# Performance work log

Measured on AMD Instinct MI355X. Metric: run time of the kernel, lower is better.

Reference implementation:

```python
import jax, jax.numpy as jnp
import numpy as np

D_MODEL = 1024
NUM_HEADS = 16
D_K = D_MODEL // NUM_HEADS
B, T = 2, 2048


def setup_inputs() -> dict:
    key = jax.random.key(0)
    ks = jax.random.split(key, 11)
    s = 1.0 / np.sqrt(D_MODEL)
    inp = {
        "q": jax.random.normal(ks[0], (B, T, D_MODEL), jnp.float32),
        "k": jax.random.normal(ks[1], (B, T, D_MODEL), jnp.float32),
        "v": jax.random.normal(ks[2], (B, T, D_MODEL), jnp.float32),
        "mask": jnp.tril(jnp.ones((1, 1, T, T), jnp.int32)),  # causal
        "wq": jax.random.normal(ks[3], (D_MODEL, D_MODEL), jnp.float32) * s,
        "bq": jnp.zeros((D_MODEL,), jnp.float32),
        "wk": jax.random.normal(ks[4], (D_MODEL, D_MODEL), jnp.float32) * s,
        "bk": jnp.zeros((D_MODEL,), jnp.float32),
        "wv": jax.random.normal(ks[5], (D_MODEL, D_MODEL), jnp.float32) * s,
        "bv": jnp.zeros((D_MODEL,), jnp.float32),
        "wo": jax.random.normal(ks[6], (D_MODEL, D_MODEL), jnp.float32) * s,
        "bo": jnp.zeros((D_MODEL,), jnp.float32),
    }
    return inp


def reference(q, k, v, mask, wq, bq, wk, bk, wv, bv, wo, bo):
    Bq, Tq, _ = q.shape
    Tk = k.shape[1]
    # projections, split into heads: (B, H, T, d_k)
    qh = (q @ wq + bq).reshape(Bq, Tq, NUM_HEADS, D_K).transpose(0, 2, 1, 3)
    kh = (k @ wk + bk).reshape(Bq, Tk, NUM_HEADS, D_K).transpose(0, 2, 1, 3)
    vh = (v @ wv + bv).reshape(Bq, Tk, NUM_HEADS, D_K).transpose(0, 2, 1, 3)
    scores = jnp.einsum("bhqd,bhkd->bhqk", qh, kh) / jnp.sqrt(jnp.float32(D_K))
    scores = jnp.where(mask == 0, jnp.float32(-1e9), scores)
    attn = jax.nn.softmax(scores, axis=-1)
    ctx = jnp.einsum("bhqk,bhkd->bhqd", attn, vh)
    ctx = ctx.transpose(0, 2, 1, 3).reshape(Bq, Tq, D_MODEL)
    return ctx @ wo + bo
```

## Files before the change

### kernel.cpp

```cpp
#include <hip/hip_runtime.h>
#include <hip/hip_bf16.h>

#define DM 1024
#define NH 16
#define DK 64
#define TT 2048
#define BATCH 2

typedef __attribute__((ext_vector_type(8))) short bf16x8;
typedef __attribute__((ext_vector_type(4))) float f32x4;
typedef __attribute__((ext_vector_type(4))) unsigned short u16x4;
typedef unsigned short u16;

__device__ inline u16 f2b(float x){ __hip_bfloat16 h = __float2bfloat16(x); return *reinterpret_cast<u16*>(&h); }

__device__ inline void gl_lds16(const u16* g, u16* l) {
  __builtin_amdgcn_global_load_lds(
      (const __attribute__((address_space(1))) unsigned int*)g,
      (__attribute__((address_space(3))) unsigned int*)l, 16, 0, 0);
}

__global__ __launch_bounds__(256) void prep(const float* __restrict__ q, const float* __restrict__ k,
                                            const float* __restrict__ v,
                                            const float* __restrict__ wq, const float* __restrict__ wk,
                                            const float* __restrict__ wv, const float* __restrict__ wo,
                                            u16* __restrict__ qb, u16* __restrict__ kb,
                                            u16* __restrict__ vb, u16* __restrict__ wt) {
  int z = blockIdx.z;
  if (z < 3) {
    const float* src = z==0 ? q : z==1 ? k : v;
    u16* dst = z==0 ? qb : z==1 ? kb : vb;
    size_t i = ((size_t)blockIdx.x*256 + threadIdx.x)*8;
    f32x4 a = *(const f32x4*)(src+i);
    f32x4 b = *(const f32x4*)(src+i+4);
    union { bf16x8 v8; u16 e[8]; } u;
    #pragma unroll
    for (int j=0;j<4;j++){ u.e[j] = f2b(a[j]); u.e[4+j] = f2b(b[j]); }
    *(bf16x8*)(dst+i) = u.v8;
  } else {
    int bx = blockIdx.x;
    if (bx >= 1024) return;
    __shared__ float tile[32][33];
    const float* src = z==3 ? wq : z==4 ? wk : z==5 ? wv : wo;
    u16* dst = wt + (size_t)(z-3)*DM*DM;
    int bxx = bx & 31, byy = bx >> 5;
    int tx = threadIdx.x & 31, ty = threadIdx.x >> 5;
    int x  = bxx*32 + tx;
    int y0 = byy*32 + ty;
    #pragma unroll
    for (int i=0;i<32;i+=8) tile[ty+i][tx] = src[(size_t)(y0+i)*DM + x];
    __syncthreads();
    int xo = byy*32 + tx;
    int yo = bxx*32 + ty;
    #pragma unroll
    for (int i=0;i<32;i+=8) dst[(size_t)(yo+i)*DM + xo] = f2b(tile[tx][ty+i]);
  }
}

__global__ __launch_bounds__(512, 2) void gemm_qkv(const u16* __restrict__ qb, const u16* __restrict__ kb,
                                                   const u16* __restrict__ vb, const u16* __restrict__ wt,
                                                   const float* __restrict__ bq, const float* __restrict__ bk,
                                                   const float* __restrict__ bv,
                                                   u16* __restrict__ qh, u16* __restrict__ kh,
                                                   u16* __restrict__ vhT) {
  const int bid = blockIdx.x;
  const int swz = (bid & 7)*24 + (bid >> 3);
  const int z  = swz >> 6;
  const int rb = swz & 63;
  const int row0 = (rb >> 2) * 256;
  const int col0 = (rb & 3) * 256;

  const u16* A = z==0 ? qb : z==1 ? kb : vb;
  const u16* W = wt + (size_t)z*DM*DM;
  const float* bias = z==0 ? bq : z==1 ? bk : bv;
  u16* outv = z==0 ? qh : z==1 ? kh : vhT;
  const int mode = (z==2);
  const float oscale = (z==0) ? 0.18033688f : 1.0f;

  __shared__ __align__(16) u16 As[2][16384];
  __shared__ __align__(16) u16 Bs[2][16384];

  const int tid = threadIdx.x, lane = tid & 63, wid = tid >> 6;
  const int li = lane & 15, quad = lane >> 4, l7 = lane & 7;
  const int wr = wid >> 2, wc = wid & 3;

  int r_[2], gs_[2];
  #pragma unroll
  for (int c=0;c<2;c++){ int idx = tid + c*512; int rr = idx>>3; int gd = idx&7; r_[c]=rr; gs_[c]=gd^(rr&7); }

  auto stage = [&](int op, int t, int hf, int slot){
    const u16* base = op ? W : A;
    const int rowbase = (op ? col0 : row0) + hf*128;
    u16* lb = (op ? Bs[slot] : As[slot]) + hf*8192;
    #pragma unroll
    for (int c=0;c<2;c++){
      gl_lds16(base + (size_t)(rowbase + r_[c])*DM + t*64 + gs_[c]*8,
               lb + ((wid*64 + c*512) << 3));
    }
  };

  f32x4 acc[8][4];
  #pragma unroll
  for (int i=0;i<8;i++)
    #pragma unroll
    for (int j=0;j<4;j++) acc[i][j] = f32x4{0.f,0.f,0.f,0.f};

  stage(1, 0, 0, 0); stage(1, 0, 1, 0);
  stage(0, 0, 0, 0); stage(0, 0, 1, 0);
  stage(1, 1, 0, 1); stage(1, 1, 1, 1);
  asm volatile("s_waitcnt vmcnt(4)" ::: "memory");
  __builtin_amdgcn_s_barrier();

  bf16x8 b[4][2];
  for (int i = 0; i < 8; i++) {
    const int t2 = 2*i;
    #pragma unroll
    for (int half = 0; half < 2; half++) {
      const int slot = half;
      #pragma unroll
      for (int q = 0; q < 4; q++) {
        if (q == 0) {
          const u16* bb = Bs[slot] + (wc>>1)*8192 + (wc&1)*4096;
          #pragma unroll
          for (int c=0;c<4;c++)
            #pragma unroll
            for (int kh=0;kh<2;kh++)
              b[c][kh] = *(const bf16x8*)&bb[(c*16 + li)*64 + ((quad + 4*kh) ^ l7)*8];
        }
        bf16x8 a[2][2];
        {
          const u16* ab = As[slot] + wr*8192;
          #pragma unroll
          for (int rr2=0; rr2<2; rr2++)
            #pragma unroll
            for (int kh=0;kh<2;kh++)
              a[rr2][kh] = *(const bf16x8*)&ab[((q*2+rr2)*16 + li)*64 + ((quad + 4*kh) ^ l7)*8];
        }
        {
          const int sop = (q >= 2);
          const int st  = t2 + 1 + half + (q >= 2);
          const int shf = q & 1;
          const int ssl = (q >= 2) ? half : (1 - half);
          if (st <= 15) stage(sop, st, shf, ssl);
        }
        if (q == 0) asm volatile("s_waitcnt lgkmcnt(8)" ::: "memory");
        __builtin_amdgcn_s_barrier();
        asm volatile("s_waitcnt lgkmcnt(0)" ::: "memory");
        __builtin_amdgcn_sched_barrier(0);
        __builtin_amdgcn_s_setprio(1);
        #pragma unroll
        for (int rr2=0; rr2<2; rr2++)
          #pragma unroll
          for (int c=0;c<4;c++)
            #pragma unroll
            for (int kh=0;kh<2;kh++)
              acc[q*2+rr2][c] = __builtin_amdgcn_mfma_f32_16x16x32_bf16(a[rr2][kh], b[c][kh], acc[q*2+rr2][c], 0,0,0);
        __builtin_amdgcn_s_setprio(0);
        if (q == 3) {
          if (half == 0) {
            if (i < 7) asm volatile("s_waitcnt vmcnt(4)" ::: "memory");
            else       asm volatile("s_waitcnt vmcnt(0)" ::: "memory");
          } else {
            if (i < 7) asm volatile("s_waitcnt vmcnt(4)" ::: "memory");
          }
        }
        __builtin_amdgcn_s_barrier();
      }
    }
  }

  if (!mode) {
    #pragma unroll
    for (int c=0;c<4;c++) {
      int col = col0 + wc*64 + c*16 + li;
      float bsv = bias[col];
      #pragma unroll
      for (int fr=0; fr<8; fr++) {
        int rowb = row0 + wr*128 + fr*16 + quad*4;
        #pragma unroll
        for (int r=0;r<4;r++)
          outv[(size_t)(rowb + r)*DM + col] = f2b((acc[fr][c][r] + bsv) * oscale);
      }
    }
  } else {
    #pragma unroll
    for (int c=0;c<4;c++) {
      int col = col0 + wc*64 + c*16 + li;
      float bsv = bias[col];
      int hh = col >> 6, d = col & 63;
      #pragma unroll
      for (int fr=0; fr<8; fr++) {
        int rowb = row0 + wr*128 + fr*16 + quad*4;
        int bb = rowb >> 11, t0 = rowb & (TT-1);
        u16x4 w;
        #pragma unroll
        for (int r=0;r<4;r++) w[r] = f2b(acc[fr][c][r] + bsv);
        *(u16x4*)&outv[(((size_t)(bb*NH + hh)*DK + d)*TT) + t0] = w;
      }
    }
  }
}

__global__ __launch_bounds__(256) void gemm_out64(const u16* __restrict__ A, const u16* __restrict__ W,
                                                  const float* __restrict__ bias, float* __restrict__ out) {
  __shared__ __align__(16) u16 As[3][128*32];
  __shared__ __align__(16) u16 Bs[3][64*32];
  const int tid = threadIdx.x, lane = tid & 63, wid = tid >> 6;
  const int li = lane & 15, quad = lane >> 4;
  const int row0 = blockIdx.x*128, col0 = blockIdx.y*64;
  const int wr = wid & 1, wc = wid >> 1;

  const int srow = lane >> 2;
  const int scol = ((lane & 3) ^ ((srow >> 1) & 3)) * 8;
  const int rsw  = (li >> 1) & 3;

  auto stage = [&](int hh, int bufi) {
    const int kk = hh*32;
    #pragma unroll
    for (int c=0;c<2;c++) {
      int ch = wid*2 + c;
      gl_lds16(A + (size_t)(row0 + ch*16 + srow)*DM + kk + scol, &As[bufi][ch*512]);
    }
    gl_lds16(W + (size_t)(col0 + wid*16 + srow)*DM + kk + scol, &Bs[bufi][wid*512]);
  };

  f32x4 acc[4][2];
  #pragma unroll
  for (int i=0;i<4;i++)
    #pragma unroll
    for (int j=0;j<2;j++) acc[i][j] = f32x4{0.f,0.f,0.f,0.f};

  stage(0, 0);
  stage(1, 1);
  asm volatile("s_waitcnt vmcnt(3)" ::: "memory");
  __builtin_amdgcn_s_barrier();

  int buf = 0;
  for (int h = 0; h < 32; h++) {
    bf16x8 a[4], b[2];
    #pragma unroll
    for (int i=0;i<4;i++) a[i] = *(const bf16x8*)&As[buf][(wr*64 + i*16 + li)*32 + (quad ^ rsw)*8];
    #pragma unroll
    for (int j=0;j<2;j++) b[j] = *(const bf16x8*)&Bs[buf][(wc*32 + j*16 + li)*32 + (quad ^ rsw)*8];

    if (h < 30) { int nb = buf + 2; if (nb >= 3) nb -= 3; stage(h+2, nb); }

    __builtin_amdgcn_s_setprio(1);
    #pragma unroll
    for (int i=0;i<4;i++)
      #pragma unroll
      for (int j=0;j<2;j++)
        acc[i][j] = __builtin_amdgcn_mfma_f32_16x16x32_bf16(a[i], b[j], acc[i][j], 0,0,0);
    __builtin_amdgcn_s_setprio(0);

    if (h < 30)       asm volatile("s_waitcnt vmcnt(3)" ::: "memory");
    else if (h == 30) asm volatile("s_waitcnt vmcnt(0)" ::: "memory");
    __builtin_amdgcn_s_barrier();
    if (++buf == 3) buf = 0;
  }

  #pragma unroll
  for (int j=0;j<2;j++) {
    int col = col0 + wc*32 + j*16 + li;
    float bsv = bias[col];
    #pragma unroll
    for (int i=0;i<4;i++) {
      #pragma unroll
      for (int r=0;r<4;r++) {
        int row = row0 + wr*64 + i*16 + quad*4 + r;
        out[(size_t)row*DM + col] = acc[i][j][r] + bsv;
      }
    }
  }
}

__global__ __launch_bounds__(256) void flash(const u16* __restrict__ qh, const u16* __restrict__ kh,
                                             const u16* __restrict__ vhT, u16* __restrict__ ctx) {
  const int bh = blockIdx.x;
  const int y  = blockIdx.y;
  const int qt = (y < 8) ? (15 - y) : (y - 8);
  const int b = bh >> 4, h = bh & 15;
  const u16* Q  = qh  + (size_t)b*TT*DM + h*DK;
  const u16* K  = kh  + (size_t)b*TT*DM + h*DK;
  const u16* Vt = vhT + (size_t)bh*DK*TT;

  const int tid = threadIdx.x, lane = tid & 63, wid = tid >> 6;
  const int li = lane & 15, quad = lane >> 4, l7 = lane & 7;

  __shared__ __align__(16) u16 Pb[4][16][64];

  const int qw0 = qt*128 + wid*32;
  const int ntw = (qw0 + 31)/64 + 1;

  bf16x8 qf[2][2];
  #pragma unroll
  for (int su=0; su<2; su++)
    #pragma unroll
    for (int k2=0; k2<2; k2++)
      qf[su][k2] = *(const bf16x8*)&Q[(size_t)(qw0 + su*16 + li)*DM + k2*32 + quad*8];

  f32x4 o[2][4];
  #pragma unroll
  for (int su=0; su<2; su++)
    #pragma unroll
    for (int d=0; d<4; d++) o[su][d] = f32x4{0.f,0.f,0.f,0.f};
  float lp[2] = {0.f, 0.f};

  for (int n = 0; n < ntw; n++) {
    const int k0 = n*64;

    f32x4 sacc[2][4];
    #pragma unroll
    for (int c=0;c<4;c++) {
      const u16* krow = &K[(size_t)(k0 + c*16 + li)*DM];
      bf16x8 kf0 = *(const bf16x8*)&krow[     quad*8];
      bf16x8 kf1 = *(const bf16x8*)&krow[32 + quad*8];
      #pragma unroll
      for (int su=0; su<2; su++) {
        f32x4 t = __builtin_amdgcn_mfma_f32_16x16x32_bf16(kf0, qf[su][0], f32x4{0.f,0.f,0.f,0.f}, 0,0,0);
        sacc[su][c] = __builtin_amdgcn_mfma_f32_16x16x32_bf16(kf1, qf[su][1], t, 0,0,0);
      }
    }

    bf16x8 vf[4][2];
    #pragma unroll
    for (int d=0; d<4; d++) {
      const u16* vrow = &Vt[(size_t)(d*16 + li)*TT + k0];
      vf[d][0] = *(const bf16x8*)&vrow[     quad*8];
      vf[d][1] = *(const bf16x8*)&vrow[32 + quad*8];
    }

    const bool dg = (k0 + 63 > qw0);
    #pragma unroll
    for (int su=0; su<2; su++) {
      const int qr = qw0 + su*16;
      if (k0 <= qr + 15) {
        const int qq = qr + li;
        float p[4][4];
        if (dg) {
          #pragma unroll
          for (int c=0;c<4;c++)
            #pragma unroll
            for (int r=0;r<4;r++){
              int key = k0 + c*16 + quad*4 + r;
              p[c][r] = (key <= qq) ? exp2f(sacc[su][c][r]) : 0.f;
            }
        } else {
          #pragma unroll
          for (int c=0;c<4;c++)
            #pragma unroll
            for (int r=0;r<4;r++)
              p[c][r] = exp2f(sacc[su][c][r]);
        }
        #pragma unroll
        for (int c=0;c<4;c++)
          #pragma unroll
          for (int r=0;r<4;r++)
            lp[su] += p[c][r];

        #pragma unroll
        for (int c=0;c<4;c++) {
          u16x4 wv;
          #pragma unroll
          for (int r=0;r<4;r++) wv[r] = f2b(p[c][r]);
          const int gc = c*2 + (quad>>1);
          *(u16x4*)&Pb[wid][li][((gc ^ l7)*8) + (quad&1)*4] = wv;
        }
        __builtin_amdgcn_wave_barrier();
        __asm__ __volatile__("s_waitcnt lgkmcnt(0)");
        bf16x8 pf0 = *(const bf16x8*)&Pb[wid][li][((quad    ) ^ l7)*8];
        bf16x8 pf1 = *(const bf16x8*)&Pb[wid][li][((quad + 4) ^ l7)*8];
        __asm__ __volatile__("s_waitcnt lgkmcnt(0)");

        #pragma unroll
        for (int d=0;d<4;d++){
          o[su][d] = __builtin_amdgcn_mfma_f32_16x16x32_bf16(vf[d][0], pf0, o[su][d], 0,0,0);
          o[su][d] = __builtin_amdgcn_mfma_f32_16x16x32_bf16(vf[d][1], pf1, o[su][d], 0,0,0);
        }
      }
    }
  }

  #pragma unroll
  for (int su=0; su<2; su++) {
    float lpv = lp[su];
    lpv += __shfl_xor(lpv, 16, 64);
    lpv += __shfl_xor(lpv, 32, 64);
    float rl = 1.0f / lpv;
    const int qq = qw0 + su*16 + li;
    #pragma unroll
    for (int d=0;d<4;d++){
      u16x4 wv;
      #pragma unroll
      for (int r=0;r<4;r++) wv[r] = f2b(o[su][d][r] * rl);
      *(u16x4*)&ctx[(size_t)(b*TT + qq)*DM + h*DK + d*16 + quad*4] = wv;
    }
  }
}

extern "C" void kernel_launch(void* const* d_in, const int* in_sizes, int n_in,
                              void* d_out, int out_size, void* d_ws, size_t ws_size,
                              hipStream_t stream) {
  const float* q   = (const float*)d_in[0];
  const float* k   = (const float*)d_in[1];
  const float* v   = (const float*)d_in[2];
  const float* wq  = (const float*)d_in[4];
  const float* bq  = (const float*)d_in[5];
  const float* wk  = (const float*)d_in[6];
  const float* bk  = (const float*)d_in[7];
  const float* wv  = (const float*)d_in[8];
  const float* bv  = (const float*)d_in[9];
  const float* wo  = (const float*)d_in[10];
  const float* bo  = (const float*)d_in[11];
  float* out = (float*)d_out;

  const size_t SZ = (size_t)BATCH*TT*DM;
  u16* wt  = (u16*)d_ws;
  u16* qb  = wt + (size_t)4*DM*DM;
  u16* kb  = qb + SZ;
  u16* vb  = kb + SZ;
  u16* qh  = vb + SZ;
  u16* kh  = qh + SZ;
  u16* vhT = kh + SZ;
  u16* ctx = qb;

  prep<<<dim3(2048, 1, 7), 256, 0, stream>>>(q, k, v, wq, wk, wv, wo, qb, kb, vb, wt);

  gemm_qkv<<<dim3(192, 1, 1), 512, 0, stream>>>(qb, kb, vb, wt, bq, bk, bv, qh, kh, vhT);

  flash<<<dim3(BATCH*NH, 16), 256, 0, stream>>>(qh, kh, vhT, ctx);

  gemm_out64<<<dim3(4096/128, DM/64), 256, 0, stream>>>(ctx, wt + (size_t)3*DM*DM, bo, out);
}
```

Before: 246.2 us.

## Stage K/V tiles in double-buffered LDS and halve flash query tile

The flash kernel now cooperatively loads each 64-key K and V^T tile into swizzled, double-buffered shared memory, prefetching the next tile into registers while computing. All four waves read from LDS instead of each issuing redundant global loads. Each wave now handles 16 query rows instead of 32, with 64-row query tiles and twice as many blocks, and MFMA sections are wrapped in s_setprio. This trades a block-wide __syncthreads per tile and extra LDS for less global traffic and better load balance.

```diff
diff --git a/kernel.cpp b/kernel.cpp
--- a/kernel.cpp
+++ b/kernel.cpp
@@ -278,7 +278,7 @@
                                              const u16* __restrict__ vhT, u16* __restrict__ ctx) {
   const int bh = blockIdx.x;
   const int y  = blockIdx.y;
-  const int qt = (y < 8) ? (15 - y) : (y - 8);
+  const int qt = (y < 16) ? (31 - y) : (y - 16);
   const int b = bh >> 4, h = bh & 15;
   const u16* Q  = qh  + (size_t)b*TT*DM + h*DK;
   const u16* K  = kh  + (size_t)b*TT*DM + h*DK;
@@ -287,114 +287,114 @@
   const int tid = threadIdx.x, lane = tid & 63, wid = tid >> 6;
   const int li = lane & 15, quad = lane >> 4, l7 = lane & 7;
 
+  __shared__ __align__(16) u16 Kl[2][4096];
+  __shared__ __align__(16) u16 Vl[2][4096];
   __shared__ __align__(16) u16 Pb[4][16][64];
 
-  const int qw0 = qt*128 + wid*32;
-  const int ntw = (qw0 + 31)/64 + 1;
-
-  bf16x8 qf[2][2];
-  #pragma unroll
-  for (int su=0; su<2; su++)
-    #pragma unroll
-    for (int k2=0; k2<2; k2++)
-      qf[su][k2] = *(const bf16x8*)&Q[(size_t)(qw0 + su*16 + li)*DM + k2*32 + quad*8];
-
-  f32x4 o[2][4];
-  #pragma unroll
-  for (int su=0; su<2; su++)
-    #pragma unroll
-    for (int d=0; d<4; d++) o[su][d] = f32x4{0.f,0.f,0.f,0.f};
-  float lp[2] = {0.f, 0.f};
-
-  for (int n = 0; n < ntw; n++) {
+  const int sr = tid >> 3;
+  const int sg = tid & 7;
+  const int ssl = (sg ^ (sr & 7)) * 8;
+
+  const int nt  = qt + 1;
+  const int qw0 = qt*64 + wid*16;
+
+  bf16x8 qf0 = *(const bf16x8*)&Q[(size_t)(qw0 + li)*DM +      quad*8];
+  bf16x8 qf1 = *(const bf16x8*)&Q[(size_t)(qw0 + li)*DM + 32 + quad*8];
+
+  f32x4 o[4];
+  #pragma unroll
+  for (int d=0; d<4; d++) o[d] = f32x4{0.f,0.f,0.f,0.f};
+  float lp = 0.f;
+
+  bf16x8 kr0 = *(const bf16x8*)&K[(size_t)(sr   )*DM + sg*8];
+  bf16x8 kr1 = *(const bf16x8*)&K[(size_t)(sr+32)*DM + sg*8];
+  bf16x8 vr0 = *(const bf16x8*)&Vt[(size_t)(sr   )*TT + sg*8];
+  bf16x8 vr1 = *(const bf16x8*)&Vt[(size_t)(sr+32)*TT + sg*8];
+
+  for (int n = 0; n < nt; n++) {
     const int k0 = n*64;
-
-    f32x4 sacc[2][4];
+    const int s = n & 1;
+    *(bf16x8*)&Kl[s][(sr   )*64 + ssl] = kr0;
+    *(bf16x8*)&Kl[s][(sr+32)*64 + ssl] = kr1;
+    *(bf16x8*)&Vl[s][(sr   )*64 + ssl] = vr0;
+    *(bf16x8*)&Vl[s][(sr+32)*64 + ssl] = vr1;
+    __syncthreads();
+    if (n+1 < nt) {
+      const int k1 = k0 + 64;
+      kr0 = *(const bf16x8*)&K[(size_t)(k1+sr   )*DM + sg*8];
+      kr1 = *(const bf16x8*)&K[(size_t)(k1+sr+32)*DM + sg*8];
+      vr0 = *(const bf16x8*)&Vt[(size_t)(sr   )*TT + k1 + sg*8];
+      vr1 = *(const bf16x8*)&Vt[(size_t)(sr+32)*TT + k1 + sg*8];
+    }
+
+    f32x4 sacc[4];
+    __builtin_amdgcn_s_setprio(1);
     #pragma unroll
     for (int c=0;c<4;c++) {
-      const u16* krow = &K[(size_t)(k0 + c*16 + li)*DM];
-      bf16x8 kf0 = *(const bf16x8*)&krow[     quad*8];
-      bf16x8 kf1 = *(const bf16x8*)&krow[32 + quad*8];
-      #pragma unroll
-      for (int su=0; su<2; su++) {
-        f32x4 t = __builtin_amdgcn_mfma_f32_16x16x32_bf16(kf0, qf[su][0], f32x4{0.f,0.f,0.f,0.f}, 0,0,0);
-        sacc[su][c] = __builtin_amdgcn_mfma_f32_16x16x32_bf16(kf1, qf[su][1], t, 0,0,0);
-      }
-    }
-
-    bf16x8 vf[4][2];
-    #pragma unroll
-    for (int d=0; d<4; d++) {
-      const u16* vrow = &Vt[(size_t)(d*16 + li)*TT + k0];
-      vf[d][0] = *(const bf16x8*)&vrow[     quad*8];
-      vf[d][1] = *(const bf16x8*)&vrow[32 + quad*8];
-    }
-
-    const bool dg = (k0 + 63 > qw0);
-    #pragma unroll
-    for (int su=0; su<2; su++) {
-      const int qr = qw0 + su*16;
-      if (k0 <= qr + 15) {
-        const int qq = qr + li;
-        float p[4][4];
-        if (dg) {
-          #pragma unroll
-          for (int c=0;c<4;c++)
-            #pragma unroll
-            for (int r=0;r<4;r++){
-              int key = k0 + c*16 + quad*4 + r;
-              p[c][r] = (key <= qq) ? exp2f(sacc[su][c][r]) : 0.f;
-            }
-        } else {
-          #pragma unroll
-          for (int c=0;c<4;c++)
-            #pragma unroll
-            for (int r=0;r<4;r++)
-              p[c][r] = exp2f(sacc[su][c][r]);
+      bf16x8 kf0 = *(const bf16x8*)&Kl[s][(c*16+li)*64 + ((quad    ) ^ l7)*8];
+      bf16x8 kf1 = *(const bf16x8*)&Kl[s][(c*16+li)*64 + ((quad + 4) ^ l7)*8];
+      f32x4 t = __builtin_amdgcn_mfma_f32_16x16x32_bf16(kf0, qf0, f32x4{0.f,0.f,0.f,0.f}, 0,0,0);
+      sacc[c] = __builtin_amdgcn_mfma_f32_16x16x32_bf16(kf1, qf1, t, 0,0,0);
+    }
+    __builtin_amdgcn_s_setprio(0);
+
+    const int qq = qw0 + li;
+    float p[4][4];
+    if (n == nt-1) {
+      #pragma unroll
+      for (int c=0;c<4;c++)
+        #pragma unroll
+        for (int r=0;r<4;r++){
+          int key = k0 + c*16 + quad*4 + r;
+          p[c][r] = (key <= qq) ? exp2f(sacc[c][r]) : 0.f;
         }
+    } else {
+      #pragma unroll
+      for (int c=0;c<4;c++)
         #pragma unroll
-        for (int c=0;c<4;c++)
-          #pragma unroll
-          for (int r=0;r<4;r++)
-            lp[su] += p[c][r];
-
-        #pragma unroll
-        for (int c=0;c<4;c++) {
-          u16x4 wv;
-          #pragma unroll
-          for (int r=0;r<4;r++) wv[r] = f2b(p[c][r]);
-          const int gc = c*2 + (quad>>1);
-          *(u16x4*)&Pb[wid][li][((gc ^ l7)*8) + (quad&1)*4] = wv;
-        }
-        __builtin_amdgcn_wave_barrier();
-        __asm__ __volatile__("s_waitcnt lgkmcnt(0)");
-        bf16x8 pf0 = *(const bf16x8*)&Pb[wid][li][((quad    ) ^ l7)*8];
-        bf16x8 pf1 = *(const bf16x8*)&Pb[wid][li][((quad + 4) ^ l7)*8];
-        __asm__ __volatile__("s_waitcnt lgkmcnt(0)");
-
-        #pragma unroll
-        for (int d=0;d<4;d++){
-          o[su][d] = __builtin_amdgcn_mfma_f32_16x16x32_bf16(vf[d][0], pf0, o[su][d], 0,0,0);
-          o[su][d] = __builtin_amdgcn_mfma_f32_16x16x32_bf16(vf[d][1], pf1, o[su][d], 0,0,0);
-        }
-      }
-    }
-  }
-
-  #pragma unroll
-  for (int su=0; su<2; su++) {
-    float lpv = lp[su];
-    lpv += __shfl_xor(lpv, 16, 64);
-    lpv += __shfl_xor(lpv, 32, 64);
-    float rl = 1.0f / lpv;
-    const int qq = qw0 + su*16 + li;
+        for (int r=0;r<4;r++)
+          p[c][r] = exp2f(sacc[c][r]);
+    }
+    #pragma unroll
+    for (int c=0;c<4;c++)
+      #pragma unroll
+      for (int r=0;r<4;r++)
+        lp += p[c][r];
+
+    #pragma unroll
+    for (int c=0;c<4;c++) {
+      u16x4 wv;
+      #pragma unroll
+      for (int r=0;r<4;r++) wv[r] = f2b(p[c][r]);
+      const int gc = c*2 + (quad>>1);
+      *(u16x4*)&Pb[wid][li][((gc ^ l7)*8) + (quad&1)*4] = wv;
+    }
+    __builtin_amdgcn_wave_barrier();
+    __asm__ __volatile__("s_waitcnt lgkmcnt(0)");
+    bf16x8 pf0 = *(const bf16x8*)&Pb[wid][li][((quad    ) ^ l7)*8];
+    bf16x8 pf1 = *(const bf16x8*)&Pb[wid][li][((quad + 4) ^ l7)*8];
+
+    __builtin_amdgcn_s_setprio(1);
     #pragma unroll
     for (int d=0;d<4;d++){
-      u16x4 wv;
-      #pragma unroll
-      for (int r=0;r<4;r++) wv[r] = f2b(o[su][d][r] * rl);
-      *(u16x4*)&ctx[(size_t)(b*TT + qq)*DM + h*DK + d*16 + quad*4] = wv;
-    }
+      bf16x8 vf0 = *(const bf16x8*)&Vl[s][(d*16+li)*64 + ((quad    ) ^ l7)*8];
+      bf16x8 vf1 = *(const bf16x8*)&Vl[s][(d*16+li)*64 + ((quad + 4) ^ l7)*8];
+      o[d] = __builtin_amdgcn_mfma_f32_16x16x32_bf16(vf0, pf0, o[d], 0,0,0);
+      o[d] = __builtin_amdgcn_mfma_f32_16x16x32_bf16(vf1, pf1, o[d], 0,0,0);
+    }
+    __builtin_amdgcn_s_setprio(0);
+  }
+
+  lp += __shfl_xor(lp, 16, 64);
+  lp += __shfl_xor(lp, 32, 64);
+  float rl = 1.0f / lp;
+  const int qq = qw0 + li;
+  #pragma unroll
+  for (int d=0;d<4;d++){
+    u16x4 wv;
+    #pragma unroll
+    for (int r=0;r<4;r++) wv[r] = f2b(o[d][r] * rl);
+    *(u16x4*)&ctx[(size_t)(b*TT + qq)*DM + h*DK + d*16 + quad*4] = wv;
   }
 }
 
@@ -428,7 +428,7 @@
 
   gemm_qkv<<<dim3(192, 1, 1), 512, 0, stream>>>(qb, kb, vb, wt, bq, bk, bv, qh, kh, vhT);
 
-  flash<<<dim3(BATCH*NH, 16), 256, 0, stream>>>(qh, kh, vhT, ctx);
+  flash<<<dim3(BATCH*NH, 32), 256, 0, stream>>>(qh, kh, vhT, ctx);
 
   gemm_out64<<<dim3(4096/128, DM/64), 256, 0, stream>>>(ctx, wt + (size_t)3*DM*DM, bo, out);
 }
```

Measured after the change: 216.9 us. -11.9%, faster.
